# Kernel optimization log

Hardware: AMD Instinct MI355X
Metric: run time of the kernel (lower is better)

## Reference

```python
import jax, jax.numpy as jnp
import numpy as np

DIM = 1024
RANK = 8
POOL = 16
SCALE = 8.0 / 8.0  # alpha / rank


def setup_inputs() -> dict:
    key = jax.random.key(0)
    ks = jax.random.split(key, 8)
    B, N = 8, 4096
    x = jax.random.normal(ks[0], (B, N, DIM), dtype=jnp.float32)
    weight = jax.random.normal(ks[1], (3 * DIM, DIM), dtype=jnp.float32) * 0.02
    bias = jax.random.normal(ks[2], (3 * DIM,), dtype=jnp.float32) * 0.02
    A_q_pool = jax.random.normal(ks[3], (POOL, DIM, RANK), dtype=jnp.float32) * 0.02
    B_q_pool = jax.random.normal(ks[4], (POOL, RANK, DIM), dtype=jnp.float32) * 0.02
    A_v_pool = jax.random.normal(ks[5], (POOL, DIM, RANK), dtype=jnp.float32) * 0.02
    B_v_pool = jax.random.normal(ks[6], (POOL, RANK, DIM), dtype=jnp.float32) * 0.02
    idx = jax.random.randint(ks[7], (B, 1), 0, POOL, dtype=jnp.int64 if jax.config.jax_enable_x64 else jnp.int32)
    frozen_mask = jnp.zeros((POOL,), dtype=bool)
    return {"x": x, "weight": weight, "bias": bias,
            "A_q_pool": A_q_pool, "B_q_pool": B_q_pool,
            "A_v_pool": A_v_pool, "B_v_pool": B_v_pool,
            "idx": idx, "frozen_mask": frozen_mask}


def _maybe_freeze(pool, i, fz):
    g = pool[i]  # [B, ., .] per-sample gather
    return jnp.where(fz, jax.lax.stop_gradient(g), g)


def reference(x, weight, bias, A_q_pool, B_q_pool, A_v_pool, B_v_pool, idx, frozen_mask):
    # Base QKV projection: [B, N, 3*dim]
    qkv = jnp.einsum('bni,oi->bno', x, weight) + bias
    i = idx[:, 0]                      # [B]
    fz = frozen_mask[i][:, None, None]  # [B,1,1]
    A_q = _maybe_freeze(A_q_pool, i, fz)  # [B, dim, rank]
    B_q = _maybe_freeze(B_q_pool, i, fz)  # [B, rank, dim]
    A_v = _maybe_freeze(A_v_pool, i, fz)
    B_v = _maybe_freeze(B_v_pool, i, fz)
    # Low-rank update: (x @ A) @ B, rank-8 bottleneck
    new_q = jnp.einsum('bnr,brj->bnj', jnp.einsum('bni,bir->bnr', x, A_q), B_q)
    new_v = jnp.einsum('bnr,brj->bnj', jnp.einsum('bni,bir->bnr', x, A_v), B_v)
    qkv = qkv.at[:, :, :DIM].add(SCALE * new_q)
    qkv = qkv.at[:, :, -DIM:].add(SCALE * new_v)
    return qkv
```

## Files before the change

### kernel.cpp

```cpp
#include <hip/hip_runtime.h>
#include <hip/hip_bf16.h>
#include <stdint.h>

#define DIM   1024
#define ODIM  3072
#define MROWS 32768
#define RANK  8
#define BK    32

typedef unsigned short u16;
typedef __attribute__((ext_vector_type(8))) short short8;
typedef __attribute__((ext_vector_type(8))) unsigned short u16x8;
typedef __attribute__((ext_vector_type(4))) unsigned short u16x4;
typedef __attribute__((ext_vector_type(4))) float f32x4;

__device__ __forceinline__ u16 f2bf(float f) {
    uint32_t u = __float_as_uint(f);
    u += 0x7fffu + ((u >> 16) & 1u);
    return (u16)(u >> 16);
}

__device__ __forceinline__ void gl2lds16(const void* g, void* l) {
    __builtin_amdgcn_global_load_lds(
        (const __attribute__((address_space(1))) void*)(uintptr_t)g,
        (__attribute__((address_space(3))) void*)(uint32_t)(uintptr_t)l,
        16, 0, 0);
}

#define BAR()    do { asm volatile("" ::: "memory"); __builtin_amdgcn_s_barrier(); asm volatile("" ::: "memory"); } while (0)
#define WAITV2() asm volatile("s_waitcnt vmcnt(2)" ::: "memory")
#define WAITV0() asm volatile("s_waitcnt vmcnt(0)" ::: "memory")

__global__ __launch_bounds__(256) void k_convert(const float* __restrict__ src,
                                                 u16* __restrict__ dst, int n) {
    const int stride = gridDim.x * blockDim.x;
    for (int t = blockIdx.x * blockDim.x + threadIdx.x; t * 8 < n; t += stride) {
        const int i = t * 8;
        float4 a = *reinterpret_cast<const float4*>(src + i);
        float4 b = *reinterpret_cast<const float4*>(src + i + 4);
        u16x8 o;
        o[0] = f2bf(a.x); o[1] = f2bf(a.y); o[2] = f2bf(a.z); o[3] = f2bf(a.w);
        o[4] = f2bf(b.x); o[5] = f2bf(b.y); o[6] = f2bf(b.z); o[7] = f2bf(b.w);
        *reinterpret_cast<u16x8*>(dst + i) = o;
    }
}

__global__ __launch_bounds__(256) void k_build(const float* __restrict__ W,
                                               const float* __restrict__ Aq_pool,
                                               const float* __restrict__ Bq_pool,
                                               const float* __restrict__ Av_pool,
                                               const float* __restrict__ Bv_pool,
                                               const int* __restrict__ idx,
                                               u16* __restrict__ Wmq,
                                               u16* __restrict__ Wmv) {
    const int b  = blockIdx.x >> 7;
    const int s  = (blockIdx.x >> 6) & 1;
    const int og = blockIdx.x & 63;
    const int p  = idx[b];
    const float* A  = (s ? Av_pool : Aq_pool) + (size_t)p * DIM * RANK;
    const float* Bp = (s ? Bv_pool : Bq_pool) + (size_t)p * RANK * DIM;
    const float* Ws = W + (size_t)(s ? 2048 : 0) * DIM;
    u16* dst = (s ? Wmv : Wmq) + (size_t)b * DIM * DIM;

    const int t  = threadIdx.x;
    const int i0 = t * 4;
    float a[4][8];
    #pragma unroll
    for (int ii = 0; ii < 4; ++ii) {
        float4 a0 = reinterpret_cast<const float4*>(A + (size_t)(i0 + ii) * RANK)[0];
        float4 a1 = reinterpret_cast<const float4*>(A + (size_t)(i0 + ii) * RANK)[1];
        a[ii][0] = a0.x; a[ii][1] = a0.y; a[ii][2] = a0.z; a[ii][3] = a0.w;
        a[ii][4] = a1.x; a[ii][5] = a1.y; a[ii][6] = a1.z; a[ii][7] = a1.w;
    }
    for (int r = 0; r < 16; ++r) {
        const int o = og * 16 + r;
        float bv[8];
        #pragma unroll
        for (int rr = 0; rr < 8; ++rr) bv[rr] = Bp[(size_t)rr * DIM + o];
        float4 w = *reinterpret_cast<const float4*>(Ws + (size_t)o * DIM + i0);
        float v[4] = {w.x, w.y, w.z, w.w};
        u16x4 ov;
        #pragma unroll
        for (int ii = 0; ii < 4; ++ii) {
            float d = 0.f;
            #pragma unroll
            for (int rr = 0; rr < 8; ++rr) d += a[ii][rr] * bv[rr];
            ov[ii] = f2bf(v[ii] + d);
        }
        *reinterpret_cast<u16x4*>(dst + (size_t)o * DIM + i0) = ov;
    }
}


__device__ __forceinline__ void stage(const u16* __restrict__ Xc,
                                      const u16* __restrict__ Bm,
                                      int m0, int nc, int tk,
                                      u16* buf, int wave, int lane) {
    const int q  = (lane & 7) ^ (lane >> 3);
    const int rl = (lane >> 3) * 2 + (q >> 2);
    const int gk = q & 3;
    const u16* ga = Xc + (size_t)(m0 + wave * 16 + rl) * DIM + tk + gk * 8;
    const u16* gb = Bm + (size_t)(nc + wave * 16 + rl) * DIM + tk + gk * 8;
    gl2lds16(ga, buf + wave * 512);
    gl2lds16(gb, buf + 8192 + wave * 512);
}

__device__ __forceinline__ void tile_mfma(const u16* __restrict__ buf,
                                          int wr, int wc, int axc,
                                          f32x4 (&acc)[4][4]) {
    short8 a[4], b[4];
    #pragma unroll
    for (int f = 0; f < 4; ++f)
        a[f] = *reinterpret_cast<const short8*>(buf + wr * 2048 + f * 512 + axc);
    #pragma unroll
    for (int n = 0; n < 4; ++n)
        b[n] = *reinterpret_cast<const short8*>(buf + 8192 + wc * 2048 + n * 512 + axc);
    __builtin_amdgcn_s_setprio(1);
    #pragma unroll
    for (int f = 0; f < 4; ++f)
        #pragma unroll
        for (int n = 0; n < 4; ++n)
            acc[f][n] = __builtin_amdgcn_mfma_f32_16x16x32_bf16(a[f], b[n], acc[f][n], 0, 0, 0);
    __builtin_amdgcn_s_setprio(0);
}

__global__ __launch_bounds__(1024, 4) void k_gemm(const u16* __restrict__ Xc,
                                                  const u16* __restrict__ Wk,
                                                  const u16* __restrict__ Wmq,
                                                  const u16* __restrict__ Wmv,
                                                  const float* __restrict__ bias,
                                                  float* __restrict__ out) {
    extern __shared__ u16 lds[];
    const int tid  = threadIdx.x;
    const int lane = tid & 63, wave = tid >> 6;
    const int wr = wave >> 2, wc = wave & 3;

    const int orig = blockIdx.x;
    const int wg   = (orig & 7) * 192 + (orig >> 3);
    const int bn   = wg % 12;
    const int bm   = wg / 12;
    const int m0 = bm * 256, n0 = bn * 256;
    const int batch = m0 >> 12;

    const u16* Bmat;
    int nc;
    if (n0 < DIM)           { Bmat = Wmq + (size_t)batch * DIM * DIM; nc = n0; }
    else if (n0 < 2 * DIM)  { Bmat = Wk;                              nc = n0 - DIM; }
    else                    { Bmat = Wmv + (size_t)batch * DIM * DIM; nc = n0 - 2 * DIM; }

    const int lr  = lane & 15;
    const int axc = (lr >> 1) * 64 + ((((lr & 1) * 4) + (lane >> 4)) ^ (lr >> 1)) * 8;

    u16* b0 = lds;
    u16* b1 = lds + 16384;
    u16* b2 = lds + 32768;

    f32x4 acc[4][4] = {};

    stage(Xc, Bmat, m0, nc, 0,  b0, wave, lane);
    stage(Xc, Bmat, m0, nc, BK, b1, wave, lane);
    WAITV2(); BAR();

    #pragma unroll 1
    for (int t3 = 0; t3 < 30; t3 += 3) {
        stage(Xc, Bmat, m0, nc, (t3 + 2) * BK, b2, wave, lane);
        tile_mfma(b0, wr, wc, axc, acc);
        WAITV2(); BAR();

        stage(Xc, Bmat, m0, nc, (t3 + 3) * BK, b0, wave, lane);
        tile_mfma(b1, wr, wc, axc, acc);
        WAITV2(); BAR();

        stage(Xc, Bmat, m0, nc, (t3 + 4) * BK, b1, wave, lane);
        tile_mfma(b2, wr, wc, axc, acc);
        WAITV2(); BAR();
    }
    tile_mfma(b0, wr, wc, axc, acc);
    WAITV0(); BAR();
    tile_mfma(b1, wr, wc, axc, acc);

    const int cn = wc * 64 + (lane & 15);
    float bcol[4];
    #pragma unroll
    for (int n = 0; n < 4; ++n) bcol[n] = bias[n0 + cn + n * 16];
    #pragma unroll
    for (int f = 0; f < 4; ++f) {
        const int rb = m0 + wr * 64 + f * 16 + (lane >> 4) * 4;
        #pragma unroll
        for (int v = 0; v < 4; ++v) {
            const size_t row = (size_t)(rb + v);
            #pragma unroll
            for (int n = 0; n < 4; ++n)
                out[row * ODIM + (size_t)(n0 + cn + n * 16)] = acc[f][n][v] + bcol[n];
        }
    }
}

extern "C" void kernel_launch(void* const* d_in, const int* in_sizes, int n_in,
                              void* d_out, int out_size, void* d_ws, size_t ws_size,
                              hipStream_t stream) {
    const float* x      = (const float*)d_in[0];
    const float* weight = (const float*)d_in[1];
    const float* bias   = (const float*)d_in[2];
    const float* Aq     = (const float*)d_in[3];
    const float* Bq     = (const float*)d_in[4];
    const float* Av     = (const float*)d_in[5];
    const float* Bv     = (const float*)d_in[6];
    const int*   idx    = (const int*)d_in[7];
    float* out = (float*)d_out;

    u16* Xc  = (u16*)d_ws;
    u16* Wk  = Xc + (size_t)MROWS * DIM;
    u16* Wmq = Wk + (size_t)DIM * DIM;
    u16* Wmv = Wmq + (size_t)8 * DIM * DIM;

    hipFuncSetAttribute(reinterpret_cast<const void*>(k_gemm),
                        hipFuncAttributeMaxDynamicSharedMemorySize, 98304);

    k_convert<<<2048, 256, 0, stream>>>(x, Xc, MROWS * DIM);
    k_convert<<<512, 256, 0, stream>>>(weight + (size_t)DIM * DIM, Wk, DIM * DIM);
    k_build<<<1024, 256, 0, stream>>>(weight, Aq, Bq, Av, Bv, idx, Wmq, Wmv);
    k_gemm<<<1536, 1024, 98304, stream>>>(Xc, Wk, Wmq, Wmv, bias, out);
}
```

Measured before the change: 321.7 us.

## Shrink GEMM tiles to 128x128 with 256-thread blocks and double buffering

Replaces the 256x256-tile, 16-wave GEMM with a 128x128-tile, 4-wave kernel using two static LDS buffers instead of three dynamic ones. The grid grows from 1536 to 6144 blocks and the swizzled block mapping is adjusted to match. The aim is more resident workgroups and simpler scheduling, including an explicit lgkmcnt wait before the MFMAs. In exchange it loses operand reuse per tile, so global/L2 traffic per FLOP roughly doubles, and prefetch depth drops to one stage with a full vmcnt(0) wait every iteration.

Measured after the change: 363.0 us. 1.13x slower.

```diff
diff --git a/kernel.cpp b/kernel.cpp
--- a/kernel.cpp
+++ b/kernel.cpp
@@ -28,8 +28,8 @@
 }
 
 #define BAR()    do { asm volatile("" ::: "memory"); __builtin_amdgcn_s_barrier(); asm volatile("" ::: "memory"); } while (0)
-#define WAITV2() asm volatile("s_waitcnt vmcnt(2)" ::: "memory")
 #define WAITV0() asm volatile("s_waitcnt vmcnt(0)" ::: "memory")
+#define WAITL0() asm volatile("s_waitcnt lgkmcnt(0)" ::: "memory")
 
 __global__ __launch_bounds__(256) void k_convert(const float* __restrict__ src,
                                                  u16* __restrict__ dst, int n) {
@@ -99,10 +99,14 @@
     const int q  = (lane & 7) ^ (lane >> 3);
     const int rl = (lane >> 3) * 2 + (q >> 2);
     const int gk = q & 3;
-    const u16* ga = Xc + (size_t)(m0 + wave * 16 + rl) * DIM + tk + gk * 8;
-    const u16* gb = Bm + (size_t)(nc + wave * 16 + rl) * DIM + tk + gk * 8;
-    gl2lds16(ga, buf + wave * 512);
-    gl2lds16(gb, buf + 8192 + wave * 512);
+    #pragma unroll
+    for (int j = 0; j < 2; ++j) {
+        const int row = wave * 32 + j * 16 + rl;
+        gl2lds16(Xc + (size_t)(m0 + row) * DIM + tk + gk * 8,
+                 buf + wave * 1024 + j * 512);
+        gl2lds16(Bm + (size_t)(nc + row) * DIM + tk + gk * 8,
+                 buf + 4096 + wave * 1024 + j * 512);
+    }
 }
 
 __device__ __forceinline__ void tile_mfma(const u16* __restrict__ buf,
@@ -114,7 +118,8 @@
         a[f] = *reinterpret_cast<const short8*>(buf + wr * 2048 + f * 512 + axc);
     #pragma unroll
     for (int n = 0; n < 4; ++n)
-        b[n] = *reinterpret_cast<const short8*>(buf + 8192 + wc * 2048 + n * 512 + axc);
+        b[n] = *reinterpret_cast<const short8*>(buf + 4096 + wc * 2048 + n * 512 + axc);
+    WAITL0();
     __builtin_amdgcn_s_setprio(1);
     #pragma unroll
     for (int f = 0; f < 4; ++f)
@@ -124,22 +129,22 @@
     __builtin_amdgcn_s_setprio(0);
 }
 
-__global__ __launch_bounds__(1024, 4) void k_gemm(const u16* __restrict__ Xc,
-                                                  const u16* __restrict__ Wk,
-                                                  const u16* __restrict__ Wmq,
-                                                  const u16* __restrict__ Wmv,
-                                                  const float* __restrict__ bias,
-                                                  float* __restrict__ out) {
-    extern __shared__ u16 lds[];
+__global__ __launch_bounds__(256, 4) void k_gemm(const u16* __restrict__ Xc,
+                                                 const u16* __restrict__ Wk,
+                                                 const u16* __restrict__ Wmq,
+                                                 const u16* __restrict__ Wmv,
+                                                 const float* __restrict__ bias,
+                                                 float* __restrict__ out) {
+    __shared__ u16 lds[2][8192];
     const int tid  = threadIdx.x;
     const int lane = tid & 63, wave = tid >> 6;
-    const int wr = wave >> 2, wc = wave & 3;
+    const int wr = wave >> 1, wc = wave & 1;
 
     const int orig = blockIdx.x;
-    const int wg   = (orig & 7) * 192 + (orig >> 3);
-    const int bn   = wg % 12;
-    const int bm   = wg / 12;
-    const int m0 = bm * 256, n0 = bn * 256;
+    const int wg   = (orig & 7) * 768 + (orig >> 3);
+    const int bn   = wg % 24;
+    const int bm   = wg / 24;
+    const int m0 = bm * 128, n0 = bn * 128;
     const int batch = m0 >> 12;
 
     const u16* Bmat;
@@ -151,33 +156,18 @@
     const int lr  = lane & 15;
     const int axc = (lr >> 1) * 64 + ((((lr & 1) * 4) + (lane >> 4)) ^ (lr >> 1)) * 8;
 
-    u16* b0 = lds;
-    u16* b1 = lds + 16384;
-    u16* b2 = lds + 32768;
-
     f32x4 acc[4][4] = {};
 
-    stage(Xc, Bmat, m0, nc, 0,  b0, wave, lane);
-    stage(Xc, Bmat, m0, nc, BK, b1, wave, lane);
-    WAITV2(); BAR();
+    stage(Xc, Bmat, m0, nc, 0, lds[0], wave, lane);
+    WAITV0(); BAR();
 
     #pragma unroll 1
-    for (int t3 = 0; t3 < 30; t3 += 3) {
-        stage(Xc, Bmat, m0, nc, (t3 + 2) * BK, b2, wave, lane);
-        tile_mfma(b0, wr, wc, axc, acc);
-        WAITV2(); BAR();
-
-        stage(Xc, Bmat, m0, nc, (t3 + 3) * BK, b0, wave, lane);
-        tile_mfma(b1, wr, wc, axc, acc);
-        WAITV2(); BAR();
-
-        stage(Xc, Bmat, m0, nc, (t3 + 4) * BK, b1, wave, lane);
-        tile_mfma(b2, wr, wc, axc, acc);
-        WAITV2(); BAR();
-    }
-    tile_mfma(b0, wr, wc, axc, acc);
-    WAITV0(); BAR();
-    tile_mfma(b1, wr, wc, axc, acc);
+    for (int t = 0; t < 31; ++t) {
+        stage(Xc, Bmat, m0, nc, (t + 1) * BK, lds[(t + 1) & 1], wave, lane);
+        tile_mfma(lds[t & 1], wr, wc, axc, acc);
+        WAITV0(); BAR();
+    }
+    tile_mfma(lds[1], wr, wc, axc, acc);
 
     const int cn = wc * 64 + (lane & 15);
     float bcol[4];
@@ -214,11 +204,8 @@
     u16* Wmq = Wk + (size_t)DIM * DIM;
     u16* Wmv = Wmq + (size_t)8 * DIM * DIM;
 
-    hipFuncSetAttribute(reinterpret_cast<const void*>(k_gemm),
-                        hipFuncAttributeMaxDynamicSharedMemorySize, 98304);
-
     k_convert<<<2048, 256, 0, stream>>>(x, Xc, MROWS * DIM);
     k_convert<<<512, 256, 0, stream>>>(weight + (size_t)DIM * DIM, Wk, DIM * DIM);
     k_build<<<1024, 256, 0, stream>>>(weight, Aq, Bq, Av, Bv, idx, Wmq, Wmv);
-    k_gemm<<<1536, 1024, 98304, stream>>>(Xc, Wk, Wmq, Wmv, bias, out);
-}
+    k_gemm<<<6144, 256, 0, stream>>>(Xc, Wk, Wmq, Wmv, bias, out);
+}
```
